# Kernel optimization log

Hardware: AMD Instinct MI355X
Metric: run time of the kernel (lower is better)

## Reference

```python
import jax, jax.numpy as jnp
import numpy as np

N_UNITS, HASH, BASIS = 32, 1024, 128
C, H, W = 3, 64, 64
D = C * H * W  # 12288
B = 16
DEPTH = 16


def setup_inputs() -> dict:
    key = jax.random.key(0)
    k0, k1, k2, k3, k4 = jax.random.split(key, 5)
    x = jax.random.normal(k0, (B, C, H, W), dtype=jnp.float32)
    P = jax.random.normal(k1, (D, HASH), dtype=jnp.float32) / np.float32(np.sqrt(D))
    basis = jax.random.normal(k2, (N_UNITS, HASH, BASIS), dtype=jnp.float32) / np.float32(np.sqrt(HASH))
    Wt = jax.random.normal(k3, (D, D), dtype=jnp.float32) / np.float32(np.sqrt(D))
    b = jax.random.normal(k4, (N_UNITS, D), dtype=jnp.float32) * 0.01
    return {"x": x, "P": P, "basis": basis, "Wt": Wt, "b": b, "depth": DEPTH}


def reference(x, P, basis, Wt, b, depth):
    """HRN routing, inference mode (all units populated).

    Returns (hashes (B, hash_feat), routes (B, depth) int32).
    """
    Bn = x.shape[0]
    n_units, hash_feat, _ = basis.shape
    xf_all = x.reshape(Bn, -1)  # (B, D)

    def one_exemplar(xf0):
        h0 = xf0 @ P  # (HASH,) hash of the exemplar
        mask0 = jnp.ones((n_units,), dtype=bool)  # units still available
        out0 = jnp.zeros((hash_feat,), dtype=xf0.dtype)

        def step(carry, _):
            xf, h, mask, out = carry
            # projection of h onto every unit's basis: (h @ B_u) @ B_u^T
            coeff = jnp.einsum('f,ufk->uk', h, basis)
            proj = jnp.einsum('uk,ufk->uf', coeff, basis)  # (n_units, HASH)
            mags = jnp.sqrt(jnp.sum(proj * proj, axis=-1))
            mags = jnp.where(mask, mags, -jnp.inf)
            idx = jnp.argmax(mags)  # routed unit
            residual = h - proj[idx]
            out = out + residual
            mask = mask.at[idx].set(False)
            # selected unit transforms the exemplar and re-hashes
            xf2 = jnp.tanh(xf @ Wt + b[idx])
            h2 = xf2 @ P
            return (xf2, h2, mask, out), idx.astype(jnp.int32)

        (_, _, _, out), route = jax.lax.scan(step, (xf0, h0, mask0, out0), None, length=depth)
        return out, route

    hashes, routes = jax.vmap(one_exemplar)(xf_all)
    return hashes, routes
```

## Files before the change

### kernel.cpp

```cpp
#include <hip/hip_runtime.h>
#include <math.h>

#define NU     32
#define HASHF  1024
#define BASISK 128
#define DD     12288
#define BN     16
#define DEPTH  16

#define KC_Y   32
#define KCH_Y  384
#define KC_H   128
#define KCH_H  96
#define LXF_LD 20

__global__ __launch_bounds__(256) void k_transpose(const float* __restrict__ x,
                                                   float* __restrict__ xfT) {
    int i = blockIdx.x * 256 + threadIdx.x;
    int b = i / DD, k = i % DD;
    xfT[(size_t)k * BN + b] = x[i];
}

__global__ __launch_bounds__(128) void k_S(const float* __restrict__ basis,
                                           float* __restrict__ S) {
    int u  = blockIdx.x >> 3;
    int it = blockIdx.x & 7;
    int t  = threadIdx.x;
    int i0 = it * 16;

    __shared__ float lrow[8 * BASISK];
    float acc[16];
#pragma unroll
    for (int i = 0; i < 16; i++) acc[i] = 0.f;

    const float* bu = basis + (size_t)u * HASHF * BASISK;
    for (int fb = 0; fb < HASHF / 8; fb++) {
#pragma unroll
        for (int r = 0; r < 8; r++)
            lrow[r * BASISK + t] = bu[(size_t)(fb * 8 + r) * BASISK + t];
        __syncthreads();
#pragma unroll
        for (int r = 0; r < 8; r++) {
            float wj = lrow[r * BASISK + t];
#pragma unroll
            for (int i = 0; i < 16; i++)
                acc[i] += lrow[r * BASISK + i0 + i] * wj;
        }
        __syncthreads();
    }
#pragma unroll
    for (int i = 0; i < 16; i++)
        S[((size_t)u * BASISK + i0 + i) * BASISK + t] = acc[i];
}

__global__ __launch_bounds__(256) void k_matP(const float* __restrict__ xfT,
                                              const float* __restrict__ P,
                                              float* __restrict__ h_part) {
    int nt = blockIdx.x & 1;
    int c  = blockIdx.x >> 1;
    int t  = threadIdx.x;
    int f0 = nt * 512 + t * 2;
    int kbase = c * KCH_H;

    __shared__ float lxf[KCH_H * BN];
    for (int j = t; j < KCH_H * BN; j += 256)
        lxf[j] = xfT[(size_t)kbase * BN + j];
    __syncthreads();

    float2 acc[BN];
#pragma unroll
    for (int b = 0; b < BN; b++) acc[b] = make_float2(0.f, 0.f);

    const float* wp = P + (size_t)kbase * HASHF + f0;
    for (int kl = 0; kl < KCH_H; kl += 8) {
        float2 w[8];
#pragma unroll
        for (int r = 0; r < 8; r++)
            w[r] = *(const float2*)(wp + (size_t)(kl + r) * HASHF);
#pragma unroll
        for (int r = 0; r < 8; r++) {
            const float4* xv = (const float4*)&lxf[(kl + r) * BN];
#pragma unroll
            for (int q = 0; q < 4; q++) {
                float4 a = xv[q];
                acc[4*q+0].x += a.x * w[r].x; acc[4*q+0].y += a.x * w[r].y;
                acc[4*q+1].x += a.y * w[r].x; acc[4*q+1].y += a.y * w[r].y;
                acc[4*q+2].x += a.z * w[r].x; acc[4*q+2].y += a.z * w[r].y;
                acc[4*q+3].x += a.w * w[r].x; acc[4*q+3].y += a.w * w[r].y;
            }
        }
    }
    float* hp = h_part + (size_t)c * (HASHF * BN) + (size_t)f0 * BN;
#pragma unroll
    for (int fi = 0; fi < 2; fi++) {
#pragma unroll
        for (int q = 0; q < 4; q++) {
            float4 v;
            v.x = fi ? acc[4*q+0].y : acc[4*q+0].x;
            v.y = fi ? acc[4*q+1].y : acc[4*q+1].x;
            v.z = fi ? acc[4*q+2].y : acc[4*q+2].x;
            v.w = fi ? acc[4*q+3].y : acc[4*q+3].x;
            *(float4*)&hp[fi * BN + q * 4] = v;
        }
    }
}

__global__ __launch_bounds__(256) void k_big(const float* __restrict__ xfT,
                                             const float* __restrict__ Wt,
                                             float* __restrict__ y_part,
                                             const float* __restrict__ h_part,
                                             const float* __restrict__ basis,
                                             float* __restrict__ coeff_part,
                                             float* __restrict__ h_full) {
    __shared__ float smem[KCH_Y * BN];
    int t = threadIdx.x;

    if (blockIdx.x < 128) {
        int u2 = blockIdx.x >> 3;
        int fc = blockIdx.x & 7;
        int u  = u2 * 2 + (t >> 7);
        int k  = t & 127;

        for (int j = t; j < 128 * BN; j += 256) {
            int fl = j >> 4, b = j & 15;
            float sum = 0.f;
            const float* hp = h_part + (size_t)(fc * 128 + fl) * BN + b;
#pragma unroll 4
            for (int c = 0; c < KC_H; c++) sum += hp[(size_t)c * (HASHF * BN)];
            smem[fl * BN + b] = sum;
            if (u2 == 0) h_full[(size_t)(fc * 128 + fl) * BN + b] = sum;
        }
        __syncthreads();

        float acc[BN];
#pragma unroll
        for (int b = 0; b < BN; b++) acc[b] = 0.f;
        const float* bp = basis + ((size_t)u * HASHF + fc * 128) * BASISK + k;
        for (int fl = 0; fl < 128; fl++) {
            float w = bp[(size_t)fl * BASISK];
            const float4* lv = (const float4*)&smem[fl * BN];
#pragma unroll
            for (int q = 0; q < 4; q++) {
                float4 a = lv[q];
                acc[4*q+0] += a.x * w;
                acc[4*q+1] += a.y * w;
                acc[4*q+2] += a.z * w;
                acc[4*q+3] += a.w * w;
            }
        }
#pragma unroll
        for (int b = 0; b < BN; b++)
            coeff_part[((size_t)(fc * BN + b) * NU + u) * BASISK + k] = acc[b];
    } else {
        int m  = blockIdx.x - 128;
        int nt = m % 24;
        int c  = m / 24;
        int n0 = nt * 512 + t * 2;
        int kbase = c * KCH_Y;

        for (int j = t; j < KCH_Y * BN; j += 256)
            smem[j] = xfT[(size_t)kbase * BN + j];
        __syncthreads();

        float2 acc[BN];
#pragma unroll
        for (int b = 0; b < BN; b++) acc[b] = make_float2(0.f, 0.f);

        const float* wp = Wt + (size_t)kbase * DD + n0;
        for (int kl = 0; kl < KCH_Y; kl += 8) {
            float2 w[8];
#pragma unroll
            for (int r = 0; r < 8; r++)
                w[r] = *(const float2*)(wp + (size_t)(kl + r) * DD);
#pragma unroll
            for (int r = 0; r < 8; r++) {
                const float4* xv = (const float4*)&smem[(kl + r) * BN];
#pragma unroll
                for (int q = 0; q < 4; q++) {
                    float4 a = xv[q];
                    acc[4*q+0].x += a.x * w[r].x; acc[4*q+0].y += a.x * w[r].y;
                    acc[4*q+1].x += a.y * w[r].x; acc[4*q+1].y += a.y * w[r].y;
                    acc[4*q+2].x += a.z * w[r].x; acc[4*q+2].y += a.z * w[r].y;
                    acc[4*q+3].x += a.w * w[r].x; acc[4*q+3].y += a.w * w[r].y;
                }
            }
        }
#pragma unroll
        for (int b = 0; b < BN; b++)
            *(float2*)&y_part[(size_t)c * (BN * DD) + (size_t)b * DD + n0] = acc[b];
    }
}

__global__ __launch_bounds__(128) void k_magsmax(const float* __restrict__ coeff_part,
                                                 const float* __restrict__ S,
                                                 float* __restrict__ coeff_full,
                                                 unsigned long long* __restrict__ best,
                                                 const int* __restrict__ routes, int s) {
    int b = blockIdx.x >> 5;
    int u = blockIdx.x & 31;
    int t = threadIdx.x;

    __shared__ int s_used;
    __shared__ float lc[BASISK];
    __shared__ float red[BASISK];

    if (t == 0) {
        int used = 0;
        for (int j = 0; j < s; j++) used |= (routes[b * DEPTH + j] == u);
        s_used = used;
    }
    __syncthreads();
    if (s_used) return;

    float cv = 0.f;
#pragma unroll
    for (int fc = 0; fc < 8; fc++)
        cv += coeff_part[((size_t)(fc * BN + b) * NU + u) * BASISK + t];
    lc[t] = cv;
    coeff_full[((size_t)b * NU + u) * BASISK + t] = cv;
    __syncthreads();

    float v = 0.f;
    const float* Sp = S + (size_t)u * BASISK * BASISK + t;
#pragma unroll 8
    for (int i = 0; i < BASISK; i++) v += Sp[(size_t)i * BASISK] * lc[i];

    red[t] = v * cv;
    __syncthreads();
    for (int st = 64; st > 0; st >>= 1) {
        if (t < st) red[t] += red[t + st];
        __syncthreads();
    }
    if (t == 0) {
        float mag = fmaxf(red[0], 0.f);
        unsigned long long key =
            ((unsigned long long)__float_as_uint(mag) << 6) |
            (unsigned long long)(31 - u);
        atomicMax(best + (size_t)s * BN + b, key);
    }
}

__global__ __launch_bounds__(256) void k_tail(const float* __restrict__ y_part,
                                              const float* __restrict__ bias,
                                              const unsigned long long* __restrict__ best,
                                              const float* __restrict__ P,
                                              float* __restrict__ xfT_next,
                                              float* __restrict__ h_part,
                                              const float* __restrict__ h_full,
                                              const float* __restrict__ coeff_full,
                                              const float* __restrict__ basis,
                                              float* __restrict__ out_acc,
                                              int* __restrict__ routes,
                                              int s, int nMatP) {
    int t = threadIdx.x;

    if ((int)blockIdx.x < nMatP) {
        __shared__ float lxf[KCH_H * LXF_LD];
        int nt = blockIdx.x & 1;
        int c  = blockIdx.x >> 1;
        int kbase = c * KCH_H;

        for (int j = t; j < KCH_H * BN; j += 256) {
            int b  = j / KCH_H;
            int fl = j - b * KCH_H;
            float sum = 0.f;
            const float* yp = y_part + (size_t)b * DD + kbase + fl;
#pragma unroll 4
            for (int cc = 0; cc < KC_Y; cc++) sum += yp[(size_t)cc * (BN * DD)];
            int u = 31 - (int)(best[(size_t)s * BN + b] & 63ull);
            float v = tanhf(sum + bias[(size_t)u * DD + kbase + fl]);
            lxf[fl * LXF_LD + b] = v;
            if (nt == (fl >= KCH_H / 2 ? 1 : 0))
                xfT_next[(size_t)(kbase + fl) * BN + b] = v;
        }
        __syncthreads();

        int f0 = nt * 512 + t * 2;
        float2 acc[BN];
#pragma unroll
        for (int b = 0; b < BN; b++) acc[b] = make_float2(0.f, 0.f);

        const float* wp = P + (size_t)kbase * HASHF + f0;
        for (int kl = 0; kl < KCH_H; kl += 8) {
            float2 w[8];
#pragma unroll
            for (int r = 0; r < 8; r++)
                w[r] = *(const float2*)(wp + (size_t)(kl + r) * HASHF);
#pragma unroll
            for (int r = 0; r < 8; r++) {
                const float4* xv = (const float4*)&lxf[(kl + r) * LXF_LD];
#pragma unroll
                for (int q = 0; q < 4; q++) {
                    float4 a = xv[q];
                    acc[4*q+0].x += a.x * w[r].x; acc[4*q+0].y += a.x * w[r].y;
                    acc[4*q+1].x += a.y * w[r].x; acc[4*q+1].y += a.y * w[r].y;
                    acc[4*q+2].x += a.z * w[r].x; acc[4*q+2].y += a.z * w[r].y;
                    acc[4*q+3].x += a.w * w[r].x; acc[4*q+3].y += a.w * w[r].y;
                }
            }
        }
        float* hp = h_part + (size_t)c * (HASHF * BN) + (size_t)f0 * BN;
#pragma unroll
        for (int fi = 0; fi < 2; fi++) {
#pragma unroll
            for (int q = 0; q < 4; q++) {
                float4 v;
                v.x = fi ? acc[4*q+0].y : acc[4*q+0].x;
                v.y = fi ? acc[4*q+1].y : acc[4*q+1].x;
                v.z = fi ? acc[4*q+2].y : acc[4*q+2].x;
                v.w = fi ? acc[4*q+3].y : acc[4*q+3].x;
                *(float4*)&hp[fi * BN + q * 4] = v;
            }
        }
    } else {
        int rid = blockIdx.x - nMatP;
        int b   = rid >> 2;
        int fq  = rid & 3;
        __shared__ float lc[BASISK];

        int u = 31 - (int)(best[(size_t)s * BN + b] & 63ull);
        if (t < BASISK) lc[t] = coeff_full[((size_t)b * NU + u) * BASISK + t];
        if (t == 0 && fq == 0) routes[b * DEPTH + s] = u;
        __syncthreads();

        int f = fq * 256 + t;
        float hv = h_full[(size_t)f * BN + b];
        const float4* br = (const float4*)&basis[((size_t)u * HASHF + f) * BASISK];
        const float4* cr = (const float4*)lc;
        float dot = 0.f;
#pragma unroll
        for (int j = 0; j < 32; j++) {
            float4 bv = br[j], c4 = cr[j];
            dot += bv.x * c4.x + bv.y * c4.y + bv.z * c4.z + bv.w * c4.w;
        }
        out_acc[b * HASHF + f] += hv - dot;
    }
}

__global__ __launch_bounds__(256) void k_out(const float* __restrict__ out_acc,
                                             const int* __restrict__ routes,
                                             float* __restrict__ o, int n) {
    int i = blockIdx.x * 256 + threadIdx.x;
    if (i >= n) return;
    if (i < BN * HASHF) o[i] = out_acc[i];
    else o[i] = (float)routes[i - BN * HASHF];
}

extern "C" void kernel_launch(void* const* d_in, const int* in_sizes, int n_in,
                              void* d_out, int out_size, void* d_ws, size_t ws_size,
                              hipStream_t stream) {
    const float* x     = (const float*)d_in[0];
    const float* P     = (const float*)d_in[1];
    const float* basis = (const float*)d_in[2];
    const float* Wt    = (const float*)d_in[3];
    const float* bias  = (const float*)d_in[4];
    float* out = (float*)d_out;

    float* w = (float*)d_ws;
    size_t off = 0;
    auto alloc = [&](size_t nf) { float* p = w + off; off += nf; return p; };

    float* xfT0       = alloc((size_t)DD * BN);
    float* xfT1       = alloc((size_t)DD * BN);
    float* out_acc    = alloc(BN * HASHF);
    unsigned long long* best = (unsigned long long*)alloc(DEPTH * BN * 2);
    float* coeff_part = alloc((size_t)8 * BN * NU * BASISK);
    float* coeff_full = alloc((size_t)BN * NU * BASISK);
    float* h_full     = alloc((size_t)HASHF * BN);
    float* S          = alloc((size_t)NU * BASISK * BASISK);
    int*   routes     = (int*)alloc(BN * DEPTH);
    float* y_part     = alloc((size_t)KC_Y * BN * DD);
    float* h_part     = alloc((size_t)KC_H * BN * HASHF);
    (void)ws_size;

    hipMemsetAsync(out_acc, 0,
                   (size_t)BN * HASHF * sizeof(float) +
                   (size_t)DEPTH * BN * sizeof(unsigned long long), stream);

    k_transpose<<<(BN * DD) / 256, 256, 0, stream>>>(x, xfT0);
    k_S<<<NU * 8, 128, 0, stream>>>(basis, S);
    k_matP<<<2 * KC_H, 256, 0, stream>>>(xfT0, P, h_part);

    for (int s = 0; s < DEPTH; s++) {
        float* cur = (s & 1) ? xfT1 : xfT0;
        float* nxt = (s & 1) ? xfT0 : xfT1;

        int nWt = (s < DEPTH - 1) ? 24 * KC_Y : 0;
        k_big<<<128 + nWt, 256, 0, stream>>>(cur, Wt, y_part, h_part, basis,
                                             coeff_part, h_full);
        k_magsmax<<<BN * NU, 128, 0, stream>>>(coeff_part, S, coeff_full, best,
                                               routes, s);
        int nMatP = (s < DEPTH - 1) ? 2 * KC_H : 0;
        k_tail<<<nMatP + 64, 256, 0, stream>>>(y_part, bias, best, P, nxt, h_part,
                                               h_full, coeff_full, basis, out_acc,
                                               routes, s, nMatP);
    }

    k_out<<<(BN * HASHF + BN * DEPTH + 255) / 256, 256, 0, stream>>>(out_acc, routes,
                                                                     out, out_size);
}
```

Baseline: 4.477 ms.

## Retile hash matmul by batch halves with float4 P loads and batch-major partials

```diff
diff --git a/kernel.cpp b/kernel.cpp
--- a/kernel.cpp
+++ b/kernel.cpp
@@ -10,9 +10,10 @@
 
 #define KC_Y   32
 #define KCH_Y  384
-#define KC_H   128
-#define KCH_H  96
-#define LXF_LD 20
+#define KC_H   64
+#define KCH_H  192
+#define LXF_LD 12
+#define CSM_LD 20
 
 __global__ __launch_bounds__(256) void k_transpose(const float* __restrict__ x,
                                                    float* __restrict__ xfT) {
@@ -56,53 +57,37 @@
 __global__ __launch_bounds__(256) void k_matP(const float* __restrict__ xfT,
                                               const float* __restrict__ P,
                                               float* __restrict__ h_part) {
-    int nt = blockIdx.x & 1;
+    int bh = blockIdx.x & 1;
     int c  = blockIdx.x >> 1;
     int t  = threadIdx.x;
-    int f0 = nt * 512 + t * 2;
     int kbase = c * KCH_H;
 
-    __shared__ float lxf[KCH_H * BN];
-    for (int j = t; j < KCH_H * BN; j += 256)
-        lxf[j] = xfT[(size_t)kbase * BN + j];
+    __shared__ __align__(16) float lxf[KCH_H * LXF_LD];
+    for (int j = t; j < KCH_H * 8; j += 256) {
+        int b_l = j & 7, fl = j >> 3;
+        lxf[fl * LXF_LD + b_l] = xfT[(size_t)(kbase + fl) * BN + bh * 8 + b_l];
+    }
     __syncthreads();
 
-    float2 acc[BN];
-#pragma unroll
-    for (int b = 0; b < BN; b++) acc[b] = make_float2(0.f, 0.f);
-
+    int f0 = t * 4;
+    float acc[8][4] = {};
     const float* wp = P + (size_t)kbase * HASHF + f0;
-    for (int kl = 0; kl < KCH_H; kl += 8) {
-        float2 w[8];
-#pragma unroll
-        for (int r = 0; r < 8; r++)
-            w[r] = *(const float2*)(wp + (size_t)(kl + r) * HASHF);
-#pragma unroll
-        for (int r = 0; r < 8; r++) {
-            const float4* xv = (const float4*)&lxf[(kl + r) * BN];
-#pragma unroll
-            for (int q = 0; q < 4; q++) {
-                float4 a = xv[q];
-                acc[4*q+0].x += a.x * w[r].x; acc[4*q+0].y += a.x * w[r].y;
-                acc[4*q+1].x += a.y * w[r].x; acc[4*q+1].y += a.y * w[r].y;
-                acc[4*q+2].x += a.z * w[r].x; acc[4*q+2].y += a.z * w[r].y;
-                acc[4*q+3].x += a.w * w[r].x; acc[4*q+3].y += a.w * w[r].y;
-            }
-        }
-    }
-    float* hp = h_part + (size_t)c * (HASHF * BN) + (size_t)f0 * BN;
-#pragma unroll
-    for (int fi = 0; fi < 2; fi++) {
-#pragma unroll
-        for (int q = 0; q < 4; q++) {
-            float4 v;
-            v.x = fi ? acc[4*q+0].y : acc[4*q+0].x;
-            v.y = fi ? acc[4*q+1].y : acc[4*q+1].x;
-            v.z = fi ? acc[4*q+2].y : acc[4*q+2].x;
-            v.w = fi ? acc[4*q+3].y : acc[4*q+3].x;
-            *(float4*)&hp[fi * BN + q * 4] = v;
-        }
-    }
+    for (int kl = 0; kl < KCH_H; kl++) {
+        float4 w = *(const float4*)(wp + (size_t)kl * HASHF);
+        const float4* xv = (const float4*)&lxf[kl * LXF_LD];
+        float4 x0 = xv[0], x1 = xv[1];
+        float xb[8] = {x0.x, x0.y, x0.z, x0.w, x1.x, x1.y, x1.z, x1.w};
+#pragma unroll
+        for (int b = 0; b < 8; b++) {
+            acc[b][0] += xb[b] * w.x; acc[b][1] += xb[b] * w.y;
+            acc[b][2] += xb[b] * w.z; acc[b][3] += xb[b] * w.w;
+        }
+    }
+    float* hp = h_part + (size_t)c * (BN * HASHF) + (size_t)(bh * 8) * HASHF + f0;
+#pragma unroll
+    for (int b = 0; b < 8; b++)
+        *(float4*)&hp[(size_t)b * HASHF] =
+            make_float4(acc[b][0], acc[b][1], acc[b][2], acc[b][3]);
 }
 
 __global__ __launch_bounds__(256) void k_big(const float* __restrict__ xfT,
@@ -112,7 +97,7 @@
                                              const float* __restrict__ basis,
                                              float* __restrict__ coeff_part,
                                              float* __restrict__ h_full) {
-    __shared__ float smem[KCH_Y * BN];
+    __shared__ __align__(16) float smem[KCH_Y * BN];
     int t = threadIdx.x;
 
     if (blockIdx.x < 128) {
@@ -122,13 +107,13 @@
         int k  = t & 127;
 
         for (int j = t; j < 128 * BN; j += 256) {
-            int fl = j >> 4, b = j & 15;
+            int b = j >> 7, fl = j & 127;
             float sum = 0.f;
-            const float* hp = h_part + (size_t)(fc * 128 + fl) * BN + b;
+            const float* hp = h_part + (size_t)b * HASHF + fc * 128 + fl;
 #pragma unroll 4
-            for (int c = 0; c < KC_H; c++) sum += hp[(size_t)c * (HASHF * BN)];
-            smem[fl * BN + b] = sum;
-            if (u2 == 0) h_full[(size_t)(fc * 128 + fl) * BN + b] = sum;
+            for (int c = 0; c < KC_H; c++) sum += hp[(size_t)c * (BN * HASHF)];
+            smem[fl * CSM_LD + b] = sum;
+            if (u2 == 0) h_full[(size_t)b * HASHF + fc * 128 + fl] = sum;
         }
         __syncthreads();
 
@@ -138,7 +123,7 @@
         const float* bp = basis + ((size_t)u * HASHF + fc * 128) * BASISK + k;
         for (int fl = 0; fl < 128; fl++) {
             float w = bp[(size_t)fl * BASISK];
-            const float4* lv = (const float4*)&smem[fl * BN];
+            const float4* lv = (const float4*)&smem[fl * CSM_LD];
 #pragma unroll
             for (int q = 0; q < 4; q++) {
                 float4 a = lv[q];
@@ -255,63 +240,45 @@
     int t = threadIdx.x;
 
     if ((int)blockIdx.x < nMatP) {
-        __shared__ float lxf[KCH_H * LXF_LD];
-        int nt = blockIdx.x & 1;
+        __shared__ __align__(16) float lxf[KCH_H * LXF_LD];
+        int bh = blockIdx.x & 1;
         int c  = blockIdx.x >> 1;
         int kbase = c * KCH_H;
 
-        for (int j = t; j < KCH_H * BN; j += 256) {
-            int b  = j / KCH_H;
-            int fl = j - b * KCH_H;
+        for (int j = t; j < KCH_H * 8; j += 256) {
+            int b_l = j / KCH_H;
+            int fl  = j - b_l * KCH_H;
+            int b   = bh * 8 + b_l;
             float sum = 0.f;
             const float* yp = y_part + (size_t)b * DD + kbase + fl;
 #pragma unroll 4
             for (int cc = 0; cc < KC_Y; cc++) sum += yp[(size_t)cc * (BN * DD)];
             int u = 31 - (int)(best[(size_t)s * BN + b] & 63ull);
             float v = tanhf(sum + bias[(size_t)u * DD + kbase + fl]);
-            lxf[fl * LXF_LD + b] = v;
-            if (nt == (fl >= KCH_H / 2 ? 1 : 0))
-                xfT_next[(size_t)(kbase + fl) * BN + b] = v;
-        }
-        __syncthreads();
-
-        int f0 = nt * 512 + t * 2;
-        float2 acc[BN];
-#pragma unroll
-        for (int b = 0; b < BN; b++) acc[b] = make_float2(0.f, 0.f);
-
+            lxf[fl * LXF_LD + b_l] = v;
+            xfT_next[(size_t)(kbase + fl) * BN + b] = v;
+        }
+        __syncthreads();
+
+        int f0 = t * 4;
+        float acc[8][4] = {};
         const float* wp = P + (size_t)kbase * HASHF + f0;
-        for (int kl = 0; kl < KCH_H; kl += 8) {
-            float2 w[8];
-#pragma unroll
-            for (int r = 0; r < 8; r++)
-                w[r] = *(const float2*)(wp + (size_t)(kl + r) * HASHF);
-#pragma unroll
-            for (int r = 0; r < 8; r++) {
-                const float4* xv = (const float4*)&lxf[(kl + r) * LXF_LD];
-#pragma unroll
-                for (int q = 0; q < 4; q++) {
-                    float4 a = xv[q];
-                    acc[4*q+0].x += a.x * w[r].x; acc[4*q+0].y += a.x * w[r].y;
-                    acc[4*q+1].x += a.y * w[r].x; acc[4*q+1].y += a.y * w[r].y;
-                    acc[4*q+2].x += a.z * w[r].x; acc[4*q+2].y += a.z * w[r].y;
-                    acc[4*q+3].x += a.w * w[r].x; acc[4*q+3].y += a.w * w[r].y;
-                }
+        for (int kl = 0; kl < KCH_H; kl++) {
+            float4 w = *(const float4*)(wp + (size_t)kl * HASHF);
+            const float4* xv = (const float4*)&lxf[kl * LXF_LD];
+            float4 x0 = xv[0], x1 = xv[1];
+            float xb[8] = {x0.x, x0.y, x0.z, x0.w, x1.x, x1.y, x1.z, x1.w};
+#pragma unroll
+            for (int b = 0; b < 8; b++) {
+                acc[b][0] += xb[b] * w.x; acc[b][1] += xb[b] * w.y;
+                acc[b][2] += xb[b] * w.z; acc[b][3] += xb[b] * w.w;
             }
         }
-        float* hp = h_part + (size_t)c * (HASHF * BN) + (size_t)f0 * BN;
-#pragma unroll
-        for (int fi = 0; fi < 2; fi++) {
-#pragma unroll
-            for (int q = 0; q < 4; q++) {
-                float4 v;
-                v.x = fi ? acc[4*q+0].y : acc[4*q+0].x;
-                v.y = fi ? acc[4*q+1].y : acc[4*q+1].x;
-                v.z = fi ? acc[4*q+2].y : acc[4*q+2].x;
-                v.w = fi ? acc[4*q+3].y : acc[4*q+3].x;
-                *(float4*)&hp[fi * BN + q * 4] = v;
-            }
-        }
+        float* hp = h_part + (size_t)c * (BN * HASHF) + (size_t)(bh * 8) * HASHF + f0;
+#pragma unroll
+        for (int b = 0; b < 8; b++)
+            *(float4*)&hp[(size_t)b * HASHF] =
+                make_float4(acc[b][0], acc[b][1], acc[b][2], acc[b][3]);
     } else {
         int rid = blockIdx.x - nMatP;
         int b   = rid >> 2;
@@ -324,7 +291,7 @@
         __syncthreads();
 
         int f = fq * 256 + t;
-        float hv = h_full[(size_t)f * BN + b];
+        float hv = h_full[(size_t)b * HASHF + f];
         const float4* br = (const float4*)&basis[((size_t)u * HASHF + f) * BASISK];
         const float4* cr = (const float4*)lc;
         float dot = 0.f;
@@ -366,7 +333,7 @@
     unsigned long long* best = (unsigned long long*)alloc(DEPTH * BN * 2);
     float* coeff_part = alloc((size_t)8 * BN * NU * BASISK);
     float* coeff_full = alloc((size_t)BN * NU * BASISK);
-    float* h_full     = alloc((size_t)HASHF * BN);
+    float* h_full     = alloc((size_t)BN * HASHF);
     float* S          = alloc((size_t)NU * BASISK * BASISK);
     int*   routes     = (int*)alloc(BN * DEPTH);
     float* y_part     = alloc((size_t)KC_Y * BN * DD);
```

New measurement: 3.795 ms. 15.2% less time.
